# Optimization experiments

Measured on AMD Instinct MI355X. Metric: run time of the kernel, lower is better.

Reference implementation:

```python
import jax, jax.numpy as jnp
import numpy as np

C_POW = 8.0  # RGLRU 'c' constant


def setup_inputs() -> dict:
    key = jax.random.key(0)
    ks = jax.random.split(key, 11)
    B, H, K, NB = 4096, 2048, 4, 4
    Hb = H // NB
    s = 1.0 / np.sqrt(H)
    sb = 1.0 / np.sqrt(Hb)
    return {
        "x": jax.random.normal(ks[0], (B, H), jnp.float32),
        "conv_state": jax.random.normal(ks[1], (B, K - 1, H), jnp.float32),
        "rglru_state": jax.random.normal(ks[2], (B, H), jnp.float32),
        "Wg": jax.random.normal(ks[3], (H, H), jnp.float32) * s,
        "Wr": jax.random.normal(ks[4], (H, H), jnp.float32) * s,
        "Wo": jax.random.normal(ks[5], (H, H), jnp.float32) * s,
        "conv_w": jax.random.normal(ks[6], (K, H), jnp.float32) * 0.5,
        "conv_b": jax.random.normal(ks[7], (H,), jnp.float32) * 0.1,
        "Wi": jax.random.normal(ks[8], (NB, Hb, Hb), jnp.float32) * sb,
        "Wrg": jax.random.normal(ks[9], (NB, Hb, Hb), jnp.float32) * sb,
        # a in (0.5, 0.99): valid base for a**(c*r) and sqrt(1 - a^2)
        "a": jax.random.uniform(ks[10], (H,), jnp.float32) * 0.49 + 0.5,
    }


def _block_linear(x, W):
    # x: [B, H], W: [NB, Hb, Hb] block-diagonal linear (torch convention y = x @ W.T per block)
    B = x.shape[0]
    NB, Hb, _ = W.shape
    xb = x.reshape(B, NB, Hb)
    yb = jnp.einsum("bnh,noh->bno", xb, W)
    return yb.reshape(B, NB * Hb)


def reference(x, conv_state, rglru_state, Wg, Wr, Wo, conv_w, conv_b, Wi, Wrg, a):
    # gate branch
    gate = jax.nn.gelu(x @ Wg.T, approximate=False)
    # recurrent branch projection
    xr = x @ Wr.T
    # depthwise causal conv single step: window = [prev K-1 inputs, current]
    window = jnp.concatenate([conv_state, xr[:, None, :]], axis=1)  # [B, K, H]
    xc = jnp.einsum("bkh,kh->bh", window, conv_w) + conv_b
    new_conv_state = window[:, 1:, :]  # [B, K-1, H]
    # RG-LRU single step
    i_t = jax.nn.sigmoid(_block_linear(xc, Wi))
    r_t = jax.nn.sigmoid(_block_linear(xc, Wrg))
    a_t = jnp.power(a, C_POW * r_t)
    multiplier = jnp.sqrt(1.0 - a_t * a_t)
    new_rglru_state = rglru_state * a_t + multiplier * (i_t * xc)
    # output projection of gated state
    out = (gate * new_rglru_state) @ Wo.T
    return out, new_conv_state, new_rglru_state
```

## Files before the change

kernel.cpp:

```cpp
#include <hip/hip_runtime.h>
#include <math.h>

#define BB 4096
#define HH 2048
#define NBK 4
#define HB 512

typedef short bh8 __attribute__((ext_vector_type(8)));
typedef float f32x4 __attribute__((ext_vector_type(4)));

__device__ __forceinline__ float gelu_exact(float v) {
    return 0.5f * v * (1.0f + erff(v * 0.70710678118654752f));
}

__device__ __forceinline__ void cvt_store(char* hiB, char* loB, int row, int cb,
                                          float4 f0, float4 f1) {
    unsigned u0 = __float_as_uint(f0.x), u1 = __float_as_uint(f0.y),
             u2 = __float_as_uint(f0.z), u3 = __float_as_uint(f0.w),
             u4 = __float_as_uint(f1.x), u5 = __float_as_uint(f1.y),
             u6 = __float_as_uint(f1.z), u7 = __float_as_uint(f1.w);
    uint4 H;
    H.x = (u1 & 0xFFFF0000u) | (u0 >> 16);
    H.y = (u3 & 0xFFFF0000u) | (u2 >> 16);
    H.z = (u5 & 0xFFFF0000u) | (u4 >> 16);
    H.w = (u7 & 0xFFFF0000u) | (u6 >> 16);
    float l0 = f0.x - __uint_as_float(u0 & 0xFFFF0000u);
    float l1 = f0.y - __uint_as_float(u1 & 0xFFFF0000u);
    float l2 = f0.z - __uint_as_float(u2 & 0xFFFF0000u);
    float l3 = f0.w - __uint_as_float(u3 & 0xFFFF0000u);
    float l4 = f1.x - __uint_as_float(u4 & 0xFFFF0000u);
    float l5 = f1.y - __uint_as_float(u5 & 0xFFFF0000u);
    float l6 = f1.z - __uint_as_float(u6 & 0xFFFF0000u);
    float l7 = f1.w - __uint_as_float(u7 & 0xFFFF0000u);
    unsigned v0 = __float_as_uint(l0), v1 = __float_as_uint(l1),
             v2 = __float_as_uint(l2), v3 = __float_as_uint(l3),
             v4 = __float_as_uint(l4), v5 = __float_as_uint(l5),
             v6 = __float_as_uint(l6), v7 = __float_as_uint(l7);
    uint4 L;
    L.x = (v1 & 0xFFFF0000u) | (v0 >> 16);
    L.y = (v3 & 0xFFFF0000u) | (v2 >> 16);
    L.z = (v5 & 0xFFFF0000u) | (v4 >> 16);
    L.w = (v7 & 0xFFFF0000u) | (v6 >> 16);
    const int s = (cb ^ ((row >> 1) & 3)) * 16;
    *(uint4*)(hiB + row * 64 + s) = H;
    *(uint4*)(loB + row * 64 + s) = L;
}

template<int EPI>
__global__ __launch_bounds__(256, 2)
void bgemm_bt(const float* __restrict__ A, int lda, long batchA,
              const float* __restrict__ Bm, int ldb, long batchB,
              float* __restrict__ C, int ldc, long batchC, int K)
{
    constexpr int BK = 32;
    __shared__ uint4 ldsv[2048];
    char* lds = (char*)ldsv;
    char* Ah = lds;
    char* Al = lds + 8192;
    char* Bh = lds + 16384;
    char* Bl = lds + 24576;

    A  += (long)blockIdx.z * batchA;
    Bm += (long)blockIdx.z * batchB;
    C  += (long)blockIdx.z * batchC;

    const int tid  = threadIdx.x;
    const int row0 = blockIdx.y * 128;
    const int col0 = blockIdx.x * 128;

    const int sr  = tid >> 2;
    const int scb = tid & 3;
    const float* Ald = A  + (long)(row0 + sr) * lda + scb * 8;
    const float* Bld = Bm + (long)(col0 + sr) * ldb + scb * 8;
    const long a64 = 64L * lda, b64 = 64L * ldb;

    const int lane = tid & 63;
    const int wr = (tid >> 7) & 1;
    const int wc = (tid >> 6) & 1;
    const int fm = lane & 15;
    const int kb = lane >> 4;
    const int slot = ((kb ^ ((fm >> 1) & 3)) & 3) * 16;
    const int aoff = (wr * 64 + fm) * 64 + slot;
    const int boff = (wc * 64 + fm) * 64 + slot;

    f32x4 acc[4][4] = {};

    float4 p0, p1, p2, p3, p4, p5, p6, p7;
    p0 = *(const float4*)(Ald);         p1 = *(const float4*)(Ald + 4);
    p2 = *(const float4*)(Ald + a64);   p3 = *(const float4*)(Ald + a64 + 4);
    p4 = *(const float4*)(Bld);         p5 = *(const float4*)(Bld + 4);
    p6 = *(const float4*)(Bld + b64);   p7 = *(const float4*)(Bld + b64 + 4);

    const int nkt = K / BK;
    for (int kt = 0; kt < nkt; ++kt) {
        __syncthreads();
        cvt_store(Ah, Al, sr,      scb, p0, p1);
        cvt_store(Ah, Al, sr + 64, scb, p2, p3);
        cvt_store(Bh, Bl, sr,      scb, p4, p5);
        cvt_store(Bh, Bl, sr + 64, scb, p6, p7);
        __syncthreads();
        if (kt + 1 < nkt) {
            const float* pa = Ald + (kt + 1) * BK;
            const float* pb = Bld + (kt + 1) * BK;
            p0 = *(const float4*)(pa);         p1 = *(const float4*)(pa + 4);
            p2 = *(const float4*)(pa + a64);   p3 = *(const float4*)(pa + a64 + 4);
            p4 = *(const float4*)(pb);         p5 = *(const float4*)(pb + 4);
            p6 = *(const float4*)(pb + b64);   p7 = *(const float4*)(pb + b64 + 4);
        }
        bh8 ahf[4], alf[4];
        #pragma unroll
        for (int i = 0; i < 4; ++i) {
            ahf[i] = *(const bh8*)(Ah + aoff + i * 1024);
            alf[i] = *(const bh8*)(Al + aoff + i * 1024);
        }
        #pragma unroll
        for (int j = 0; j < 4; ++j) {
            const bh8 bhf = *(const bh8*)(Bh + boff + j * 1024);
            const bh8 blf = *(const bh8*)(Bl + boff + j * 1024);
            #pragma unroll
            for (int i = 0; i < 4; ++i)
                acc[i][j] = __builtin_amdgcn_mfma_f32_16x16x32_bf16(ahf[i], bhf, acc[i][j], 0, 0, 0);
            #pragma unroll
            for (int i = 0; i < 4; ++i)
                acc[i][j] = __builtin_amdgcn_mfma_f32_16x16x32_bf16(ahf[i], blf, acc[i][j], 0, 0, 0);
            #pragma unroll
            for (int i = 0; i < 4; ++i)
                acc[i][j] = __builtin_amdgcn_mfma_f32_16x16x32_bf16(alf[i], bhf, acc[i][j], 0, 0, 0);
        }
    }

    const int erow = row0 + wr * 64 + (lane >> 4) * 4;
    const int ecol = col0 + wc * 64 + fm;
    #pragma unroll
    for (int i = 0; i < 4; ++i)
        #pragma unroll
        for (int j = 0; j < 4; ++j)
            #pragma unroll
            for (int r = 0; r < 4; ++r) {
                float v = acc[i][j][r];
                if (EPI == 1) v = gelu_exact(v);
                C[(long)(erow + i * 16 + r) * ldc + ecol + j * 16] = v;
            }
}

__global__ void conv_kernel(const float* __restrict__ cs,
                            const float* __restrict__ xr,
                            const float* __restrict__ cw,
                            const float* __restrict__ cb,
                            float* __restrict__ xc,
                            float* __restrict__ ncs)
{
    const long idx = (long)blockIdx.x * blockDim.x + threadIdx.x;
    const long n4 = (long)BB * HH / 4;
    if (idx >= n4) return;
    const long b = idx / (HH / 4);
    const int  h = (int)(idx % (HH / 4)) * 4;

    const float4 c0 = *(const float4*)&cs[(b * 3 + 0) * HH + h];
    const float4 c1 = *(const float4*)&cs[(b * 3 + 1) * HH + h];
    const float4 c2 = *(const float4*)&cs[(b * 3 + 2) * HH + h];
    const float4 xv = *(const float4*)&xr[b * HH + h];
    const float4 w0 = *(const float4*)&cw[0 * HH + h];
    const float4 w1 = *(const float4*)&cw[1 * HH + h];
    const float4 w2 = *(const float4*)&cw[2 * HH + h];
    const float4 w3 = *(const float4*)&cw[3 * HH + h];
    const float4 bb = *(const float4*)&cb[h];

    float4 r;
    r.x = fmaf(c0.x, w0.x, fmaf(c1.x, w1.x, fmaf(c2.x, w2.x, fmaf(xv.x, w3.x, bb.x))));
    r.y = fmaf(c0.y, w0.y, fmaf(c1.y, w1.y, fmaf(c2.y, w2.y, fmaf(xv.y, w3.y, bb.y))));
    r.z = fmaf(c0.z, w0.z, fmaf(c1.z, w1.z, fmaf(c2.z, w2.z, fmaf(xv.z, w3.z, bb.z))));
    r.w = fmaf(c0.w, w0.w, fmaf(c1.w, w1.w, fmaf(c2.w, w2.w, fmaf(xv.w, w3.w, bb.w))));

    *(float4*)&xc[b * HH + h] = r;
    *(float4*)&ncs[(b * 3 + 0) * HH + h] = c1;
    *(float4*)&ncs[(b * 3 + 1) * HH + h] = c2;
    *(float4*)&ncs[(b * 3 + 2) * HH + h] = xv;
}

__device__ __forceinline__ float4 sigmoid4(float4 v) {
    v.x = 1.0f / (1.0f + expf(-v.x));
    v.y = 1.0f / (1.0f + expf(-v.y));
    v.z = 1.0f / (1.0f + expf(-v.z));
    v.w = 1.0f / (1.0f + expf(-v.w));
    return v;
}

__global__ void rglru_kernel(const float* __restrict__ yi,
                             const float* __restrict__ yr,
                             const float* __restrict__ xc,
                             const float* __restrict__ rg,
                             const float* __restrict__ av,
                             const float* __restrict__ gate,
                             float* __restrict__ nrs,
                             float* __restrict__ hbuf)
{
    const long idx = (long)blockIdx.x * blockDim.x + threadIdx.x;
    const long n4 = (long)BB * HH / 4;
    if (idx >= n4) return;
    const long b = idx / (HH / 4);
    const int  h = (int)(idx % (HH / 4)) * 4;
    const long off = b * HH + h;

    const float4 i4 = sigmoid4(*(const float4*)&yi[off]);
    const float4 r4 = sigmoid4(*(const float4*)&yr[off]);
    const float4 x4 = *(const float4*)&xc[off];
    const float4 s4 = *(const float4*)&rg[off];
    const float4 a4 = *(const float4*)&av[h];
    const float4 g4 = *(const float4*)&gate[off];

    float4 at, o, hh;
    at.x = expf(8.0f * r4.x * logf(a4.x));
    at.y = expf(8.0f * r4.y * logf(a4.y));
    at.z = expf(8.0f * r4.z * logf(a4.z));
    at.w = expf(8.0f * r4.w * logf(a4.w));

    o.x = fmaf(s4.x, at.x, sqrtf(fmaxf(0.0f, 1.0f - at.x * at.x)) * (i4.x * x4.x));
    o.y = fmaf(s4.y, at.y, sqrtf(fmaxf(0.0f, 1.0f - at.y * at.y)) * (i4.y * x4.y));
    o.z = fmaf(s4.z, at.z, sqrtf(fmaxf(0.0f, 1.0f - at.z * at.z)) * (i4.z * x4.z));
    o.w = fmaf(s4.w, at.w, sqrtf(fmaxf(0.0f, 1.0f - at.w * at.w)) * (i4.w * x4.w));

    hh.x = g4.x * o.x; hh.y = g4.y * o.y; hh.z = g4.z * o.z; hh.w = g4.w * o.w;

    *(float4*)&nrs[off]  = o;
    *(float4*)&hbuf[off] = hh;
}

extern "C" void kernel_launch(void* const* d_in, const int* in_sizes, int n_in,
                              void* d_out, int out_size, void* d_ws, size_t ws_size,
                              hipStream_t stream) {
    const float* x    = (const float*)d_in[0];
    const float* cs   = (const float*)d_in[1];
    const float* rg   = (const float*)d_in[2];
    const float* Wg   = (const float*)d_in[3];
    const float* Wr   = (const float*)d_in[4];
    const float* Wo   = (const float*)d_in[5];
    const float* cw   = (const float*)d_in[6];
    const float* cb   = (const float*)d_in[7];
    const float* Wi   = (const float*)d_in[8];
    const float* Wrg  = (const float*)d_in[9];
    const float* av   = (const float*)d_in[10];

    const long BH = (long)BB * HH;
    float* out = (float*)d_out;
    float* ncs = out + BH;
    float* nrs = out + 4 * BH;

    float* ws   = (float*)d_ws;
    float* gate = ws;
    float* xr   = ws + BH;
    float* xc   = ws + 2 * BH;
    float* yi   = xr;
    float* yr   = out;

    const dim3 blk(256);
    const dim3 g1(HH / 128, BB / 128, 1);
    const dim3 g2(HB / 128, BB / 128, NBK);
    const int nElem4 = (int)(BH / 4);
    const dim3 ge((nElem4 + 255) / 256);

    bgemm_bt<1><<<g1, blk, 0, stream>>>(x, HH, 0, Wg, HH, 0, gate, HH, 0, HH);
    bgemm_bt<0><<<g1, blk, 0, stream>>>(x, HH, 0, Wr, HH, 0, xr, HH, 0, HH);
    conv_kernel<<<ge, blk, 0, stream>>>(cs, xr, cw, cb, xc, ncs);
    bgemm_bt<0><<<g2, blk, 0, stream>>>(xc, HH, HB, Wi, HB, (long)HB * HB, yi, HH, HB, HB);
    bgemm_bt<0><<<g2, blk, 0, stream>>>(xc, HH, HB, Wrg, HB, (long)HB * HB, yr, HH, HB, HB);
    rglru_kernel<<<ge, blk, 0, stream>>>(yi, yr, xc, rg, av, gate, nrs, gate);
    bgemm_bt<0><<<g1, blk, 0, stream>>>(gate, HH, 0, Wo, HH, 0, out, HH, 0, HH);
}
```

Before: 722.0 us.

## Double-buffer GEMM LDS tiles and fuse block-diagonal GEMMs with RG-LRU epilogue

```diff
diff --git a/kernel.cpp b/kernel.cpp
--- a/kernel.cpp
+++ b/kernel.cpp
@@ -53,12 +53,8 @@
               float* __restrict__ C, int ldc, long batchC, int K)
 {
     constexpr int BK = 32;
-    __shared__ uint4 ldsv[2048];
+    __shared__ uint4 ldsv[4096];
     char* lds = (char*)ldsv;
-    char* Ah = lds;
-    char* Al = lds + 8192;
-    char* Bh = lds + 16384;
-    char* Bl = lds + 24576;
 
     A  += (long)blockIdx.z * batchA;
     Bm += (long)blockIdx.z * batchB;
@@ -90,15 +86,16 @@
     p2 = *(const float4*)(Ald + a64);   p3 = *(const float4*)(Ald + a64 + 4);
     p4 = *(const float4*)(Bld);         p5 = *(const float4*)(Bld + 4);
     p6 = *(const float4*)(Bld + b64);   p7 = *(const float4*)(Bld + b64 + 4);
+    cvt_store(lds,         lds + 8192,  sr,      scb, p0, p1);
+    cvt_store(lds,         lds + 8192,  sr + 64, scb, p2, p3);
+    cvt_store(lds + 16384, lds + 24576, sr,      scb, p4, p5);
+    cvt_store(lds + 16384, lds + 24576, sr + 64, scb, p6, p7);
+    __syncthreads();
 
     const int nkt = K / BK;
     for (int kt = 0; kt < nkt; ++kt) {
-        __syncthreads();
-        cvt_store(Ah, Al, sr,      scb, p0, p1);
-        cvt_store(Ah, Al, sr + 64, scb, p2, p3);
-        cvt_store(Bh, Bl, sr,      scb, p4, p5);
-        cvt_store(Bh, Bl, sr + 64, scb, p6, p7);
-        __syncthreads();
+        const int cur = (kt & 1) << 15;
+        const int nxt = cur ^ 32768;
         if (kt + 1 < nkt) {
             const float* pa = Ald + (kt + 1) * BK;
             const float* pb = Bld + (kt + 1) * BK;
@@ -107,6 +104,8 @@
             p4 = *(const float4*)(pb);         p5 = *(const float4*)(pb + 4);
             p6 = *(const float4*)(pb + b64);   p7 = *(const float4*)(pb + b64 + 4);
         }
+        char* Ah = lds + cur;          char* Al = Ah + 8192;
+        char* Bh = lds + cur + 16384;  char* Bl = Bh + 8192;
         bh8 ahf[4], alf[4];
         #pragma unroll
         for (int i = 0; i < 4; ++i) {
@@ -127,6 +126,13 @@
             for (int i = 0; i < 4; ++i)
                 acc[i][j] = __builtin_amdgcn_mfma_f32_16x16x32_bf16(alf[i], bhf, acc[i][j], 0, 0, 0);
         }
+        if (kt + 1 < nkt) {
+            cvt_store(lds + nxt,         lds + nxt + 8192,  sr,      scb, p0, p1);
+            cvt_store(lds + nxt,         lds + nxt + 8192,  sr + 64, scb, p2, p3);
+            cvt_store(lds + nxt + 16384, lds + nxt + 24576, sr,      scb, p4, p5);
+            cvt_store(lds + nxt + 16384, lds + nxt + 24576, sr + 64, scb, p6, p7);
+        }
+        __syncthreads();
     }
 
     const int erow = row0 + wr * 64 + (lane >> 4) * 4;
@@ -141,6 +147,124 @@
                 if (EPI == 1) v = gelu_exact(v);
                 C[(long)(erow + i * 16 + r) * ldc + ecol + j * 16] = v;
             }
+}
+
+__global__ __launch_bounds__(256, 2)
+void bd_rglru(const float* __restrict__ xc,
+              const float* __restrict__ Wi,
+              const float* __restrict__ Wrg,
+              const float* __restrict__ rg,
+              const float* __restrict__ gate,
+              const float* __restrict__ av,
+              float* __restrict__ nrs,
+              float* __restrict__ hbuf)
+{
+    constexpr int BK = 32;
+    __shared__ uint4 ldsv[3072];
+    char* lds = (char*)ldsv;
+    char* Ah = lds;          char* Al = lds + 8192;
+    char* Ih = lds + 16384;  char* Il = lds + 24576;
+    char* Rh = lds + 32768;  char* Rl = lds + 40960;
+
+    const int nb   = blockIdx.z;
+    const int tid  = threadIdx.x;
+    const int row0 = blockIdx.y * 128;
+    const int col0 = blockIdx.x * 128;
+
+    const int sr  = tid >> 2;
+    const int scb = tid & 3;
+    const float* Ald = xc  + (long)(row0 + sr) * HH + nb * HB + scb * 8;
+    const float* Ild = Wi  + (long)nb * HB * HB + (long)(col0 + sr) * HB + scb * 8;
+    const float* Rld = Wrg + (long)nb * HB * HB + (long)(col0 + sr) * HB + scb * 8;
+    const long a64 = 64L * HH;
+    const long w64 = 64L * HB;
+
+    const int lane = tid & 63;
+    const int wr = (tid >> 7) & 1;
+    const int wc = (tid >> 6) & 1;
+    const int fm = lane & 15;
+    const int kb = lane >> 4;
+    const int slot = ((kb ^ ((fm >> 1) & 3)) & 3) * 16;
+    const int aoff = (wr * 64 + fm) * 64 + slot;
+    const int boff = (wc * 64 + fm) * 64 + slot;
+
+    f32x4 ai[4][4] = {}, ar[4][4] = {};
+
+    for (int kt = 0; kt < HB / BK; ++kt) {
+        const int ko = kt * BK;
+        const float4 a0 = *(const float4*)(Ald + ko);
+        const float4 a1 = *(const float4*)(Ald + ko + 4);
+        const float4 a2 = *(const float4*)(Ald + a64 + ko);
+        const float4 a3 = *(const float4*)(Ald + a64 + ko + 4);
+        const float4 i0 = *(const float4*)(Ild + ko);
+        const float4 i1 = *(const float4*)(Ild + ko + 4);
+        const float4 i2 = *(const float4*)(Ild + w64 + ko);
+        const float4 i3 = *(const float4*)(Ild + w64 + ko + 4);
+        const float4 r0 = *(const float4*)(Rld + ko);
+        const float4 r1 = *(const float4*)(Rld + ko + 4);
+        const float4 r2 = *(const float4*)(Rld + w64 + ko);
+        const float4 r3 = *(const float4*)(Rld + w64 + ko + 4);
+        __syncthreads();
+        cvt_store(Ah, Al, sr,      scb, a0, a1);
+        cvt_store(Ah, Al, sr + 64, scb, a2, a3);
+        cvt_store(Ih, Il, sr,      scb, i0, i1);
+        cvt_store(Ih, Il, sr + 64, scb, i2, i3);
+        cvt_store(Rh, Rl, sr,      scb, r0, r1);
+        cvt_store(Rh, Rl, sr + 64, scb, r2, r3);
+        __syncthreads();
+        bh8 ahf[4], alf[4];
+        #pragma unroll
+        for (int i = 0; i < 4; ++i) {
+            ahf[i] = *(const bh8*)(Ah + aoff + i * 1024);
+            alf[i] = *(const bh8*)(Al + aoff + i * 1024);
+        }
+        #pragma unroll
+        for (int j = 0; j < 4; ++j) {
+            const bh8 bihf = *(const bh8*)(Ih + boff + j * 1024);
+            const bh8 bilf = *(const bh8*)(Il + boff + j * 1024);
+            const bh8 brhf = *(const bh8*)(Rh + boff + j * 1024);
+            const bh8 brlf = *(const bh8*)(Rl + boff + j * 1024);
+            #pragma unroll
+            for (int i = 0; i < 4; ++i)
+                ai[i][j] = __builtin_amdgcn_mfma_f32_16x16x32_bf16(ahf[i], bihf, ai[i][j], 0, 0, 0);
+            #pragma unroll
+            for (int i = 0; i < 4; ++i)
+                ai[i][j] = __builtin_amdgcn_mfma_f32_16x16x32_bf16(ahf[i], bilf, ai[i][j], 0, 0, 0);
+            #pragma unroll
+            for (int i = 0; i < 4; ++i)
+                ai[i][j] = __builtin_amdgcn_mfma_f32_16x16x32_bf16(alf[i], bihf, ai[i][j], 0, 0, 0);
+            #pragma unroll
+            for (int i = 0; i < 4; ++i)
+                ar[i][j] = __builtin_amdgcn_mfma_f32_16x16x32_bf16(ahf[i], brhf, ar[i][j], 0, 0, 0);
+            #pragma unroll
+            for (int i = 0; i < 4; ++i)
+                ar[i][j] = __builtin_amdgcn_mfma_f32_16x16x32_bf16(ahf[i], brlf, ar[i][j], 0, 0, 0);
+            #pragma unroll
+            for (int i = 0; i < 4; ++i)
+                ar[i][j] = __builtin_amdgcn_mfma_f32_16x16x32_bf16(alf[i], brhf, ar[i][j], 0, 0, 0);
+        }
+    }
+
+    const int erow = row0 + wr * 64 + (lane >> 4) * 4;
+    const int ecolL = col0 + wc * 64 + fm;
+    #pragma unroll
+    for (int j = 0; j < 4; ++j) {
+        const int gcol = nb * HB + ecolL + j * 16;
+        const float la8 = 8.0f * logf(av[gcol]);
+        #pragma unroll
+        for (int i = 0; i < 4; ++i)
+            #pragma unroll
+            for (int r = 0; r < 4; ++r) {
+                const long off = (long)(erow + i * 16 + r) * HH + gcol;
+                const float it = 1.0f / (1.0f + expf(-ai[i][j][r]));
+                const float rt = 1.0f / (1.0f + expf(-ar[i][j][r]));
+                const float at = expf(la8 * rt);
+                const float mult = sqrtf(fmaxf(0.0f, 1.0f - at * at));
+                const float o = fmaf(rg[off], at, mult * (it * xc[off]));
+                nrs[off]  = o;
+                hbuf[off] = gate[off] * o;
+            }
+    }
 }
 
 __global__ void conv_kernel(const float* __restrict__ cs,
@@ -176,54 +300,6 @@
     *(float4*)&ncs[(b * 3 + 0) * HH + h] = c1;
     *(float4*)&ncs[(b * 3 + 1) * HH + h] = c2;
     *(float4*)&ncs[(b * 3 + 2) * HH + h] = xv;
-}
-
-__device__ __forceinline__ float4 sigmoid4(float4 v) {
-    v.x = 1.0f / (1.0f + expf(-v.x));
-    v.y = 1.0f / (1.0f + expf(-v.y));
-    v.z = 1.0f / (1.0f + expf(-v.z));
-    v.w = 1.0f / (1.0f + expf(-v.w));
-    return v;
-}
-
-__global__ void rglru_kernel(const float* __restrict__ yi,
-                             const float* __restrict__ yr,
-                             const float* __restrict__ xc,
-                             const float* __restrict__ rg,
-                             const float* __restrict__ av,
-                             const float* __restrict__ gate,
-                             float* __restrict__ nrs,
-                             float* __restrict__ hbuf)
-{
-    const long idx = (long)blockIdx.x * blockDim.x + threadIdx.x;
-    const long n4 = (long)BB * HH / 4;
-    if (idx >= n4) return;
-    const long b = idx / (HH / 4);
-    const int  h = (int)(idx % (HH / 4)) * 4;
-    const long off = b * HH + h;
-
-    const float4 i4 = sigmoid4(*(const float4*)&yi[off]);
-    const float4 r4 = sigmoid4(*(const float4*)&yr[off]);
-    const float4 x4 = *(const float4*)&xc[off];
-    const float4 s4 = *(const float4*)&rg[off];
-    const float4 a4 = *(const float4*)&av[h];
-    const float4 g4 = *(const float4*)&gate[off];
-
-    float4 at, o, hh;
-    at.x = expf(8.0f * r4.x * logf(a4.x));
-    at.y = expf(8.0f * r4.y * logf(a4.y));
-    at.z = expf(8.0f * r4.z * logf(a4.z));
-    at.w = expf(8.0f * r4.w * logf(a4.w));
-
-    o.x = fmaf(s4.x, at.x, sqrtf(fmaxf(0.0f, 1.0f - at.x * at.x)) * (i4.x * x4.x));
-    o.y = fmaf(s4.y, at.y, sqrtf(fmaxf(0.0f, 1.0f - at.y * at.y)) * (i4.y * x4.y));
-    o.z = fmaf(s4.z, at.z, sqrtf(fmaxf(0.0f, 1.0f - at.z * at.z)) * (i4.z * x4.z));
-    o.w = fmaf(s4.w, at.w, sqrtf(fmaxf(0.0f, 1.0f - at.w * at.w)) * (i4.w * x4.w));
-
-    hh.x = g4.x * o.x; hh.y = g4.y * o.y; hh.z = g4.z * o.z; hh.w = g4.w * o.w;
-
-    *(float4*)&nrs[off]  = o;
-    *(float4*)&hbuf[off] = hh;
 }
 
 extern "C" void kernel_launch(void* const* d_in, const int* in_sizes, int n_in,
@@ -250,8 +326,6 @@
     float* gate = ws;
     float* xr   = ws + BH;
     float* xc   = ws + 2 * BH;
-    float* yi   = xr;
-    float* yr   = out;
 
     const dim3 blk(256);
     const dim3 g1(HH / 128, BB / 128, 1);
@@ -262,8 +336,6 @@
     bgemm_bt<1><<<g1, blk, 0, stream>>>(x, HH, 0, Wg, HH, 0, gate, HH, 0, HH);
     bgemm_bt<0><<<g1, blk, 0, stream>>>(x, HH, 0, Wr, HH, 0, xr, HH, 0, HH);
     conv_kernel<<<ge, blk, 0, stream>>>(cs, xr, cw, cb, xc, ncs);
-    bgemm_bt<0><<<g2, blk, 0, stream>>>(xc, HH, HB, Wi, HB, (long)HB * HB, yi, HH, HB, HB);
-    bgemm_bt<0><<<g2, blk, 0, stream>>>(xc, HH, HB, Wrg, HB, (long)HB * HB, yr, HH, HB, HB);
-    rglru_kernel<<<ge, blk, 0, stream>>>(yi, yr, xc, rg, av, gate, nrs, gate);
+    bd_rglru<<<g2, blk, 0, stream>>>(xc, Wi, Wrg, rg, gate, av, nrs, gate);
     bgemm_bt<0><<<g1, blk, 0, stream>>>(gate, HH, 0, Wo, HH, 0, out, HH, 0, HH);
 }
```

Measured after the change: 859.0 us. 19.0% more time.
